# Kernel tuning notes

Measured on AMD Instinct MI355X. Metric: run time of the kernel, lower is better.

The kernel has to match this reference:

```python
import jax, jax.numpy as jnp
import numpy as np

KS = (5, 5, 5)      # dilated_kernel_size (Kd, Kh, Kw)
STRIDE = (1, 1, 1)
PADDING = (2, 2, 2)
GROUPS = 1


def construct_kernel(W, P, ks):
    # W: (oc, ic/g, kc), P: (3, oc, ic/g, kc)
    Kd, Kh, Kw = ks
    lim = jnp.floor_divide(jnp.array([Kd, Kh, Kw], dtype=P.dtype), 2.0)
    Pp = P + lim[:, None, None, None]          # shift to grid coords
    Pf = jnp.floor(Pp)
    R = Pp - Pf                                # fractional parts, (3, oc, ic, kc)
    P1, P2, P3 = Pf[0], Pf[1], Pf[2]
    R1, R2, R3 = R[0], R[1], R[2]
    # trilinear weights factorize per axis. In the torch original:
    #   L (depth axis, Kd)  compares against P1/R1
    #   I (width axis, Kw)  compares against P2/R2
    #   J (height axis, Kh) compares against P3/R3
    gL = jnp.arange(Kd, dtype=P.dtype)[:, None, None, None]
    gJ = jnp.arange(Kh, dtype=P.dtype)[:, None, None, None]
    gI = jnp.arange(Kw, dtype=P.dtype)[:, None, None, None]
    aL = (gL == P1) * (1.0 - R1) + (gL == P1 + 1.0) * R1   # (Kd, oc, ic, kc)
    aJ = (gJ == P3) * (1.0 - R3) + (gJ == P3 + 1.0) * R3   # (Kh, oc, ic, kc)
    aI = (gI == P2) * (1.0 - R2) + (gI == P2 + 1.0) * R2   # (Kw, oc, ic, kc)
    # K[o,c,l,j,i] = sum_k W[o,c,k] * aL[l,o,c,k] * aJ[j,o,c,k] * aI[i,o,c,k]
    K = jnp.einsum('ock,lock,jock,iock->oclji', W, aL, aJ, aI)
    return K  # (oc, ic/g, Kd, Kh, Kw)


def setup_inputs() -> dict:
    key = jax.random.key(0)
    k1, k2, k3, k4 = jax.random.split(key, 4)
    x = jax.random.normal(k1, (2, 32, 16, 32, 32), dtype=jnp.float32)
    weight = jax.random.normal(k2, (64, 32, 16), dtype=jnp.float32) * 0.05
    P = jax.random.normal(k3, (3, 64, 32, 16), dtype=jnp.float32) * 0.5
    bias = jax.random.normal(k4, (64,), dtype=jnp.float32) * 0.05
    return {"x": x, "weight": weight, "P": P, "bias": bias}


def reference(x, weight, P, bias):
    K = construct_kernel(weight, P, KS)
    out = jax.lax.conv_general_dilated(
        x, K,
        window_strides=STRIDE,
        padding=[(p, p) for p in PADDING],
        dimension_numbers=('NCDHW', 'OIDHW', 'NCDHW'),
        feature_group_count=GROUPS,
    )
    return out + bias[None, :, None, None, None]
```

## Files before the change

kernel.cpp:

```cpp
#include <hip/hip_runtime.h>

#define OC 64
#define IC 32
#define KC 16

typedef __attribute__((ext_vector_type(8))) short bf16x8;
typedef __attribute__((ext_vector_type(16))) float f32x16;

__device__ inline unsigned short f2bf(float f) {
    unsigned u = __builtin_bit_cast(unsigned, f);
    unsigned r = (u + 0x7fffu + ((u >> 16) & 1u)) >> 16;
    return (unsigned short)r;
}

__global__ __launch_bounds__(128) void prep(const float* __restrict__ x,
                                            const float* __restrict__ W,
                                            const float* __restrict__ P,
                                            short* __restrict__ xp,
                                            short* __restrict__ Kb) {
    const int b = blockIdx.x;
    if (b < 1440) {
        const int n = b / 720;
        const int rem = b - n * 720;
        const int z = rem / 36;
        const int h = rem - z * 36;
        const int zr = z - 2, hr = h - 2;
        short* orow = xp + (size_t)((n * 20 + z) * 36 + h) * 1152;

        if ((unsigned)zr >= 16u || (unsigned)hr >= 32u) {
            for (int idx = threadIdx.x; idx < 144; idx += 128)
                *reinterpret_cast<float4*>(orow + idx * 8) =
                    make_float4(0.f, 0.f, 0.f, 0.f);
            return;
        }

        __shared__ float sR[32][36];
        const float* xb = x + ((size_t)(n * 32) * 16 + zr) * 1024 + hr * 32;
        for (int idx = threadIdx.x; idx < 32 * 36; idx += 128) {
            const int c = idx / 36;
            const int w = idx - c * 36;
            const int wr = w - 2;
            float v = 0.f;
            if ((unsigned)wr < 32u) v = xb[(size_t)c * 16384 + wr];
            sR[c][w] = v;
        }
        __syncthreads();
        for (int idx = threadIdx.x; idx < 144; idx += 128) {
            const int cg = idx / 36;
            const int w  = idx - cg * 36;
            bf16x8 pk;
            #pragma unroll
            for (int e = 0; e < 8; ++e) pk[e] = (short)f2bf(sR[cg * 8 + e][w]);
            *reinterpret_cast<bf16x8*>(orow + idx * 8) = pk;
        }
    } else {
        const int pair = b - 1440;
        const int o = pair >> 5;
        const int c = pair & 31;
        const int cell = threadIdx.x;
        if (cell >= 125) return;
        const int l = cell / 25;
        const int j = (cell / 5) % 5;
        const int i = cell % 5;
        const float fl = (float)l, fj = (float)j, fi = (float)i;
        const int base = (o * IC + c) * KC;
        float acc = 0.f;
        #pragma unroll
        for (int k = 0; k < KC; ++k) {
            const float w  = W[base + k];
            const float p1 = P[0 * OC * IC * KC + base + k] + 2.0f;
            const float p2 = P[1 * OC * IC * KC + base + k] + 2.0f;
            const float p3 = P[2 * OC * IC * KC + base + k] + 2.0f;
            const float f1 = floorf(p1), r1 = p1 - f1;
            const float f2 = floorf(p2), r2 = p2 - f2;
            const float f3 = floorf(p3), r3 = p3 - f3;
            const float wl = (fl == f1) ? (1.f - r1) : ((fl == f1 + 1.f) ? r1 : 0.f);
            const float wj = (fj == f3) ? (1.f - r3) : ((fj == f3 + 1.f) ? r3 : 0.f);
            const float wi = (fi == f2) ? (1.f - r2) : ((fi == f2 + 1.f) ? r2 : 0.f);
            acc += w * (wl * wj * wi);
        }
        const int og = o >> 5;
        Kb[(size_t)(og * 125 + cell) * 1024 + (c >> 3) * 256 + (o & 31) * 8 + (c & 7)] =
            (short)f2bf(acc);
    }
}

#define ASLOT 25600
#define BBASE 51200
#define BSLOT 13824

__global__ __launch_bounds__(512, 1) void conv_mfma(const short* __restrict__ Kb,
                                                    const short* __restrict__ xp,
                                                    const float* __restrict__ bias,
                                                    float* __restrict__ out) {
    const int sw = (blockIdx.x & 7) * 32 + (blockIdx.x >> 3);
    const int og = sw & 1;
    const int hb = (sw >> 1) & 3;
    const int d  = (sw >> 3) & 15;
    const int n  = sw >> 7;
    const int h0 = hb * 8;

    __shared__ short sL[2 * ASLOT + 2 * BSLOT];

    const int tid  = threadIdx.x;
    const int wv   = tid >> 6;
    const int hp   = wv >> 1;
    const int g    = wv & 1;
    const int lane = tid & 63;
    const int wcol = lane & 31;
    const int hi   = lane >> 5;

    const short* srcA0 = Kb + (size_t)(og * 125) * 1024;
    const short* srcB0 = xp + ((size_t)(n * 20 + d) * 36 + h0) * 1152;

    const int aoff = wcol * 8 + (g * 2 + hi) * 256;
    const int boff = (g * 2 + hi) * 288 + wcol * 8;

    f32x16 acc0, acc1;
    for (int e = 0; e < 16; ++e) { acc0[e] = 0.f; acc1[e] = 0.f; }

    bf16x8 Aq[3][5];
    bf16x8 Bq[3][5];

#define STAGEA(L, BUF)                                                        \
    {                                                                         \
        const short* s_ = srcA0 + (size_t)(L) * 25600;                        \
        short* d_ = sL + (BUF) * ASLOT;                                       \
        _Pragma("unroll")                                                     \
        for (int k_ = 0; k_ < 6; ++k_) {                                      \
            const int t_ = k_ * 512 + tid;                                    \
            __builtin_amdgcn_global_load_lds(                                 \
                (const __attribute__((address_space(1))) unsigned int*)(s_ + t_ * 8), \
                (__attribute__((address_space(3))) unsigned int*)(d_ + t_ * 8), \
                16, 0, 0);                                                    \
        }                                                                     \
        if (tid < 128) {                                                      \
            const int t_ = 3072 + tid;                                        \
            __builtin_amdgcn_global_load_lds(                                 \
                (const __attribute__((address_space(1))) unsigned int*)(s_ + t_ * 8), \
                (__attribute__((address_space(3))) unsigned int*)(d_ + t_ * 8), \
                16, 0, 0);                                                    \
        }                                                                     \
    }

#define STAGEB(L, BUF)                                                        \
    {                                                                         \
        const short* s_ = srcB0 + (size_t)(L) * 41472;                        \
        short* d_ = sL + BBASE + (BUF) * BSLOT;                               \
        _Pragma("unroll")                                                     \
        for (int k_ = 0; k_ < 3; ++k_) {                                      \
            const int t_ = k_ * 512 + tid;                                    \
            __builtin_amdgcn_global_load_lds(                                 \
                (const __attribute__((address_space(1))) unsigned int*)(s_ + t_ * 8), \
                (__attribute__((address_space(3))) unsigned int*)(d_ + t_ * 8), \
                16, 0, 0);                                                    \
        }                                                                     \
        if (tid < 192) {                                                      \
            const int t_ = 1536 + tid;                                        \
            __builtin_amdgcn_global_load_lds(                                 \
                (const __attribute__((address_space(1))) unsigned int*)(s_ + t_ * 8), \
                (__attribute__((address_space(3))) unsigned int*)(d_ + t_ * 8), \
                16, 0, 0);                                                    \
        }                                                                     \
    }

#define LOADA(S, BUF, J)                                                      \
    {                                                                         \
        const short* pa_ = sL + (BUF) * ASLOT + (J) * 5120 + aoff;            \
        _Pragma("unroll")                                                     \
        for (int i_ = 0; i_ < 5; ++i_)                                        \
            Aq[S][i_] = *reinterpret_cast<const bf16x8*>(pa_ + i_ * 1024);    \
    }

#define LOADB(S, BUF, K)                                                      \
    {                                                                         \
        const short* pb_ = sL + BBASE + (BUF) * BSLOT + (2 * hp + (K)) * 1152 + boff; \
        _Pragma("unroll")                                                     \
        for (int i_ = 0; i_ < 5; ++i_)                                        \
            Bq[S][i_] = *reinterpret_cast<const bf16x8*>(pb_ + i_ * 8);       \
    }

#define MFMA_STEP(RA, S0, S1)                                                 \
    {                                                                         \
        __builtin_amdgcn_s_setprio(1);                                        \
        _Pragma("unroll")                                                     \
        for (int i_ = 0; i_ < 5; ++i_) {                                      \
            acc0 = __builtin_amdgcn_mfma_f32_32x32x16_bf16(Aq[RA][i_], Bq[S0][i_], acc0, 0, 0, 0); \
            acc1 = __builtin_amdgcn_mfma_f32_32x32x16_bf16(Aq[RA][i_], Bq[S1][i_], acc1, 0, 0, 0); \
        }                                                                     \
        __builtin_amdgcn_s_setprio(0);                                        \
    }

    STAGEA(0, 0);
    STAGEB(0, 0);
    __syncthreads();

    #pragma unroll
    for (int l = 0; l < 5; ++l) {
        const int buf = l & 1;
        if (l < 4) { STAGEA(l + 1, buf ^ 1); STAGEB(l + 1, buf ^ 1); }
        LOADA(0, buf, 0); LOADA(1, buf, 1);
        LOADB(0, buf, 0); LOADB(1, buf, 1);
        #pragma unroll
        for (int j = 0; j < 5; ++j) {
            if (j < 3) LOADA((j + 2) % 3, buf, j + 2);
            if (j < 4) LOADB((j + 2) % 3, buf, j + 2);
            MFMA_STEP(j % 3, j % 3, (j + 1) % 3);
        }
        if (l < 4) __syncthreads();
    }

#undef STAGEA
#undef STAGEB
#undef LOADA
#undef LOADB
#undef MFMA_STEP

    __syncthreads();
    float* sF = reinterpret_cast<float*>(sL);
    if (g == 1) {
        #pragma unroll
        for (int e = 0; e < 16; ++e) {
            sF[hp * 2048 + e * 64 + lane]        = acc0[e];
            sF[hp * 2048 + (e + 16) * 64 + lane] = acc1[e];
        }
    }
    __syncthreads();
    if (g == 0) {
        const int h = h0 + 2 * hp;
        #pragma unroll
        for (int reg = 0; reg < 16; ++reg) {
            const int o = og * 32 + (reg & 3) + 8 * (reg >> 2) + 4 * hi;
            const float bo = bias[o];
            float* op = out + (((size_t)(n * 64 + o) * 16 + d) * 32 + h) * 32 + wcol;
            op[0]  = acc0[reg] + sF[hp * 2048 + reg * 64 + lane] + bo;
            op[32] = acc1[reg] + sF[hp * 2048 + (reg + 16) * 64 + lane] + bo;
        }
    }
}

extern "C" void kernel_launch(void* const* d_in, const int* in_sizes, int n_in,
                              void* d_out, int out_size, void* d_ws, size_t ws_size,
                              hipStream_t stream) {
    const float* x    = (const float*)d_in[0];
    const float* W    = (const float*)d_in[1];
    const float* P    = (const float*)d_in[2];
    const float* bias = (const float*)d_in[3];
    float* outp = (float*)d_out;

    short* Kb = (short*)d_ws;
    short* xp = (short*)((char*)d_ws + 524288);

    prep<<<1440 + 2048, 128, 0, stream>>>(x, W, P, xp, Kb);
    conv_mfma<<<256, 512, 0, stream>>>(Kb, xp, bias, outp);
}
```

Baseline: 27.02 us.

## Reassign conv waves to 4 output rows with kw-split, batch prep blocks

The conv kernel now gives each wave four output rows with four accumulators and splits the kw taps 3/2 across wave pairs, so each A fragment is reused across four B rows instead of two. The partial sums from four waves are reduced through LDS in the epilogue, and every wave writes one output row. The prep kernel packs two units per 256-thread block, reads x with float4 loads and stages W/P in shared memory. The risks are a larger LDS reduction, more accumulator registers, and an uneven 3/2 kw split between waves.

```diff
diff --git a/kernel.cpp b/kernel.cpp
--- a/kernel.cpp
+++ b/kernel.cpp
@@ -13,75 +13,92 @@
     return (unsigned short)r;
 }
 
-__global__ __launch_bounds__(128) void prep(const float* __restrict__ x,
+__global__ __launch_bounds__(256) void prep(const float* __restrict__ x,
                                             const float* __restrict__ W,
                                             const float* __restrict__ P,
                                             short* __restrict__ xp,
                                             short* __restrict__ Kb) {
-    const int b = blockIdx.x;
-    if (b < 1440) {
-        const int n = b / 720;
-        const int rem = b - n * 720;
+    __shared__ float sR[2][32][36];
+    __shared__ float sWP[2][64];
+    const int tid = threadIdx.x;
+    const int u   = tid >> 7;
+    const int ut  = tid & 127;
+    const int b   = blockIdx.x;
+
+    if (b < 720) {
+        const int ub = b * 2 + u;
+        const int n = ub / 720;
+        const int rem = ub - n * 720;
         const int z = rem / 36;
         const int h = rem - z * 36;
         const int zr = z - 2, hr = h - 2;
         short* orow = xp + (size_t)((n * 20 + z) * 36 + h) * 1152;
-
-        if ((unsigned)zr >= 16u || (unsigned)hr >= 32u) {
-            for (int idx = threadIdx.x; idx < 144; idx += 128)
+        const bool edge = ((unsigned)zr >= 16u) || ((unsigned)hr >= 32u);
+
+        if (!edge) {
+            const float* xb = x + ((size_t)(n * 32) * 16 + zr) * 1024 + hr * 32;
+            #pragma unroll
+            for (int k = 0; k < 2; ++k) {
+                const int id = ut + k * 128;
+                const int c = id >> 3, w4 = id & 7;
+                const float4 v = *reinterpret_cast<const float4*>(xb + c * 16384 + w4 * 4);
+                float* dst = &sR[u][c][2 + w4 * 4];
+                *reinterpret_cast<float2*>(dst)     = make_float2(v.x, v.y);
+                *reinterpret_cast<float2*>(dst + 2) = make_float2(v.z, v.w);
+            }
+            {
+                const int c = ut >> 2, wz = ut & 3;
+                const int w = (wz < 2) ? wz : 32 + wz;
+                sR[u][c][w] = 0.f;
+            }
+        }
+        __syncthreads();
+        if (edge) {
+            for (int idx = ut; idx < 144; idx += 128)
                 *reinterpret_cast<float4*>(orow + idx * 8) =
                     make_float4(0.f, 0.f, 0.f, 0.f);
-            return;
-        }
-
-        __shared__ float sR[32][36];
-        const float* xb = x + ((size_t)(n * 32) * 16 + zr) * 1024 + hr * 32;
-        for (int idx = threadIdx.x; idx < 32 * 36; idx += 128) {
-            const int c = idx / 36;
-            const int w = idx - c * 36;
-            const int wr = w - 2;
-            float v = 0.f;
-            if ((unsigned)wr < 32u) v = xb[(size_t)c * 16384 + wr];
-            sR[c][w] = v;
-        }
-        __syncthreads();
-        for (int idx = threadIdx.x; idx < 144; idx += 128) {
-            const int cg = idx / 36;
-            const int w  = idx - cg * 36;
-            bf16x8 pk;
-            #pragma unroll
-            for (int e = 0; e < 8; ++e) pk[e] = (short)f2bf(sR[cg * 8 + e][w]);
-            *reinterpret_cast<bf16x8*>(orow + idx * 8) = pk;
+        } else {
+            for (int idx = ut; idx < 144; idx += 128) {
+                const int cg = idx / 36;
+                const int w  = idx - cg * 36;
+                bf16x8 pk;
+                #pragma unroll
+                for (int e = 0; e < 8; ++e) pk[e] = (short)f2bf(sR[u][cg * 8 + e][w]);
+                *reinterpret_cast<bf16x8*>(orow + idx * 8) = pk;
+            }
         }
     } else {
-        const int pair = b - 1440;
-        const int o = pair >> 5;
-        const int c = pair & 31;
-        const int cell = threadIdx.x;
-        if (cell >= 125) return;
-        const int l = cell / 25;
-        const int j = (cell / 5) % 5;
-        const int i = cell % 5;
-        const float fl = (float)l, fj = (float)j, fi = (float)i;
-        const int base = (o * IC + c) * KC;
-        float acc = 0.f;
-        #pragma unroll
-        for (int k = 0; k < KC; ++k) {
-            const float w  = W[base + k];
-            const float p1 = P[0 * OC * IC * KC + base + k] + 2.0f;
-            const float p2 = P[1 * OC * IC * KC + base + k] + 2.0f;
-            const float p3 = P[2 * OC * IC * KC + base + k] + 2.0f;
-            const float f1 = floorf(p1), r1 = p1 - f1;
-            const float f2 = floorf(p2), r2 = p2 - f2;
-            const float f3 = floorf(p3), r3 = p3 - f3;
-            const float wl = (fl == f1) ? (1.f - r1) : ((fl == f1 + 1.f) ? r1 : 0.f);
-            const float wj = (fj == f3) ? (1.f - r3) : ((fj == f3 + 1.f) ? r3 : 0.f);
-            const float wi = (fi == f2) ? (1.f - r2) : ((fi == f2 + 1.f) ? r2 : 0.f);
-            acc += w * (wl * wj * wi);
+        const int pair = (b - 720) * 2 + u;
+        if (ut < 64)
+            sWP[u][ut] = (ut < 16) ? W[pair * 16 + ut]
+                                   : P[((ut >> 4) - 1) * 32768 + pair * 16 + (ut & 15)];
+        __syncthreads();
+        if (ut < 125) {
+            const int cell = ut;
+            const int l = cell / 25;
+            const int j = (cell / 5) % 5;
+            const int i = cell % 5;
+            const float fl = (float)l, fj = (float)j, fi = (float)i;
+            float acc = 0.f;
+            #pragma unroll
+            for (int k = 0; k < KC; ++k) {
+                const float w  = sWP[u][k];
+                const float p1 = sWP[u][16 + k] + 2.0f;
+                const float p2 = sWP[u][32 + k] + 2.0f;
+                const float p3 = sWP[u][48 + k] + 2.0f;
+                const float f1 = floorf(p1), r1 = p1 - f1;
+                const float f2 = floorf(p2), r2 = p2 - f2;
+                const float f3 = floorf(p3), r3 = p3 - f3;
+                const float wl = (fl == f1) ? (1.f - r1) : ((fl == f1 + 1.f) ? r1 : 0.f);
+                const float wj = (fj == f3) ? (1.f - r3) : ((fj == f3 + 1.f) ? r3 : 0.f);
+                const float wi = (fi == f2) ? (1.f - r2) : ((fi == f2 + 1.f) ? r2 : 0.f);
+                acc += w * (wl * wj * wi);
+            }
+            const int o = pair >> 5, c = pair & 31;
+            const int og = o >> 5;
+            Kb[(size_t)(og * 125 + cell) * 1024 + (c >> 3) * 256 + (o & 31) * 8 + (c & 7)] =
+                (short)f2bf(acc);
         }
-        const int og = o >> 5;
-        Kb[(size_t)(og * 125 + cell) * 1024 + (c >> 3) * 256 + (o & 31) * 8 + (c & 7)] =
-            (short)f2bf(acc);
     }
 }
 
@@ -89,7 +106,7 @@
 #define BBASE 51200
 #define BSLOT 13824
 
-__global__ __launch_bounds__(512, 1) void conv_mfma(const short* __restrict__ Kb,
+__global__ __launch_bounds__(512, 2) void conv_mfma(const short* __restrict__ Kb,
                                                     const short* __restrict__ xp,
                                                     const float* __restrict__ bias,
                                                     float* __restrict__ out) {
@@ -104,23 +121,26 @@
 
     const int tid  = threadIdx.x;
     const int wv   = tid >> 6;
-    const int hp   = wv >> 1;
-    const int g    = wv & 1;
     const int lane = tid & 63;
     const int wcol = lane & 31;
     const int hi   = lane >> 5;
+    const int hp   = wv >> 2;
+    const int g    = (wv >> 1) & 1;
+    const int s    = (wv ^ (wv >> 2)) & 1;
 
     const short* srcA0 = Kb + (size_t)(og * 125) * 1024;
     const short* srcB0 = xp + ((size_t)(n * 20 + d) * 36 + h0) * 1152;
 
     const int aoff = wcol * 8 + (g * 2 + hi) * 256;
     const int boff = (g * 2 + hi) * 288 + wcol * 8;
-
-    f32x16 acc0, acc1;
-    for (int e = 0; e < 16; ++e) { acc0[e] = 0.f; acc1[e] = 0.f; }
-
-    bf16x8 Aq[3][5];
-    bf16x8 Bq[3][5];
+    const int rb   = 4 * hp;
+
+    f32x16 ac0, ac1, ac2, ac3;
+    #pragma unroll
+    for (int e = 0; e < 16; ++e) { ac0[e] = 0.f; ac1[e] = 0.f; ac2[e] = 0.f; ac3[e] = 0.f; }
+
+    bf16x8 Aq[2][3];
+    bf16x8 Bq[5][3];
 
 #define STAGEA(L, BUF)                                                        \
     {                                                                         \
@@ -164,78 +184,91 @@
         }                                                                     \
     }
 
-#define LOADA(S, BUF, J)                                                      \
-    {                                                                         \
-        const short* pa_ = sL + (BUF) * ASLOT + (J) * 5120 + aoff;            \
-        _Pragma("unroll")                                                     \
-        for (int i_ = 0; i_ < 5; ++i_)                                        \
-            Aq[S][i_] = *reinterpret_cast<const bf16x8*>(pa_ + i_ * 1024);    \
-    }
-
-#define LOADB(S, BUF, K)                                                      \
-    {                                                                         \
-        const short* pb_ = sL + BBASE + (BUF) * BSLOT + (2 * hp + (K)) * 1152 + boff; \
-        _Pragma("unroll")                                                     \
-        for (int i_ = 0; i_ < 5; ++i_)                                        \
-            Bq[S][i_] = *reinterpret_cast<const bf16x8*>(pb_ + i_ * 8);       \
-    }
-
-#define MFMA_STEP(RA, S0, S1)                                                 \
+#define LOADA(PAR, BUF, J, I0, NI)                                            \
+    {                                                                         \
+        const short* pa_ = sL + (BUF) * ASLOT + ((J) * 5 + (I0)) * 1024 + aoff; \
+        _Pragma("unroll")                                                     \
+        for (int ii = 0; ii < (NI); ++ii)                                     \
+            Aq[PAR][ii] = *reinterpret_cast<const bf16x8*>(pa_ + ii * 1024);  \
+    }
+
+#define LOADB(SLOT, BUF, RW, I0, NI)                                          \
+    {                                                                         \
+        const short* pb_ = sL + BBASE + (BUF) * BSLOT + (rb + (RW)) * 1152 + boff + (I0) * 8; \
+        _Pragma("unroll")                                                     \
+        for (int ii = 0; ii < (NI); ++ii)                                     \
+            Bq[SLOT][ii] = *reinterpret_cast<const bf16x8*>(pb_ + ii * 8);    \
+    }
+
+#define MFMA_STEP(J, NI)                                                      \
     {                                                                         \
         __builtin_amdgcn_s_setprio(1);                                        \
         _Pragma("unroll")                                                     \
-        for (int i_ = 0; i_ < 5; ++i_) {                                      \
-            acc0 = __builtin_amdgcn_mfma_f32_32x32x16_bf16(Aq[RA][i_], Bq[S0][i_], acc0, 0, 0, 0); \
-            acc1 = __builtin_amdgcn_mfma_f32_32x32x16_bf16(Aq[RA][i_], Bq[S1][i_], acc1, 0, 0, 0); \
+        for (int ii = 0; ii < (NI); ++ii) {                                   \
+            const bf16x8 a_ = Aq[(J) & 1][ii];                                \
+            ac0 = __builtin_amdgcn_mfma_f32_32x32x16_bf16(a_, Bq[(J) % 5][ii], ac0, 0, 0, 0);       \
+            ac1 = __builtin_amdgcn_mfma_f32_32x32x16_bf16(a_, Bq[((J) + 1) % 5][ii], ac1, 0, 0, 0); \
+            ac2 = __builtin_amdgcn_mfma_f32_32x32x16_bf16(a_, Bq[((J) + 2) % 5][ii], ac2, 0, 0, 0); \
+            ac3 = __builtin_amdgcn_mfma_f32_32x32x16_bf16(a_, Bq[((J) + 3) % 5][ii], ac3, 0, 0, 0); \
         }                                                                     \
         __builtin_amdgcn_s_setprio(0);                                        \
     }
 
-    STAGEA(0, 0);
-    STAGEB(0, 0);
-    __syncthreads();
-
-    #pragma unroll
-    for (int l = 0; l < 5; ++l) {
-        const int buf = l & 1;
-        if (l < 4) { STAGEA(l + 1, buf ^ 1); STAGEB(l + 1, buf ^ 1); }
-        LOADA(0, buf, 0); LOADA(1, buf, 1);
-        LOADB(0, buf, 0); LOADB(1, buf, 1);
-        #pragma unroll
-        for (int j = 0; j < 5; ++j) {
-            if (j < 3) LOADA((j + 2) % 3, buf, j + 2);
-            if (j < 4) LOADB((j + 2) % 3, buf, j + 2);
-            MFMA_STEP(j % 3, j % 3, (j + 1) % 3);
-        }
-        if (l < 4) __syncthreads();
-    }
+#define MAIN(I0, NI)                                                          \
+    {                                                                         \
+        STAGEA(0, 0); STAGEB(0, 0);                                           \
+        __syncthreads();                                                      \
+        _Pragma("unroll")                                                     \
+        for (int l = 0; l < 5; ++l) {                                         \
+            const int buf = l & 1;                                            \
+            if (l < 4) { STAGEA(l + 1, buf ^ 1); STAGEB(l + 1, buf ^ 1); }    \
+            LOADA(0, buf, 0, I0, NI);                                         \
+            LOADB(0, buf, 0, I0, NI);                                         \
+            LOADB(1, buf, 1, I0, NI);                                         \
+            LOADB(2, buf, 2, I0, NI);                                         \
+            LOADB(3, buf, 3, I0, NI);                                         \
+            _Pragma("unroll")                                                 \
+            for (int j = 0; j < 5; ++j) {                                     \
+                if (j < 4) {                                                  \
+                    LOADA((j + 1) & 1, buf, j + 1, I0, NI);                   \
+                    LOADB((j + 4) % 5, buf, j + 4, I0, NI);                   \
+                }                                                             \
+                MFMA_STEP(j, NI);                                             \
+            }                                                                 \
+            if (l < 4) __syncthreads();                                       \
+        }                                                                     \
+    }
+
+    if (s == 0) { MAIN(0, 3) } else { MAIN(3, 2) }
 
 #undef STAGEA
 #undef STAGEB
 #undef LOADA
 #undef LOADB
 #undef MFMA_STEP
+#undef MAIN
 
     __syncthreads();
     float* sF = reinterpret_cast<float*>(sL);
-    if (g == 1) {
+    const int wbase = (g * 2 + s) * 2 + hp;
+#define WR(R, A)                                                              \
+    { _Pragma("unroll")                                                       \
+      for (int e = 0; e < 16; ++e)                                            \
+          sF[((wbase * 4 + (R)) * 16 + e) * 64 + lane] = A[e]; }
+    WR(0, ac0) WR(1, ac1) WR(2, ac2) WR(3, ac3)
+#undef WR
+    __syncthreads();
+
+    const int hpR = wv >> 2, rR = wv & 3;
+    const int h = h0 + wv;
+    #pragma unroll
+    for (int e = 0; e < 16; ++e) {
+        float v = 0.f;
         #pragma unroll
-        for (int e = 0; e < 16; ++e) {
-            sF[hp * 2048 + e * 64 + lane]        = acc0[e];
-            sF[hp * 2048 + (e + 16) * 64 + lane] = acc1[e];
-        }
-    }
-    __syncthreads();
-    if (g == 0) {
-        const int h = h0 + 2 * hp;
-        #pragma unroll
-        for (int reg = 0; reg < 16; ++reg) {
-            const int o = og * 32 + (reg & 3) + 8 * (reg >> 2) + 4 * hi;
-            const float bo = bias[o];
-            float* op = out + (((size_t)(n * 64 + o) * 16 + d) * 32 + h) * 32 + wcol;
-            op[0]  = acc0[reg] + sF[hp * 2048 + reg * 64 + lane] + bo;
-            op[32] = acc1[reg] + sF[hp * 2048 + (reg + 16) * 64 + lane] + bo;
-        }
+        for (int q = 0; q < 4; ++q)
+            v += sF[(((q * 2 + hpR) * 4 + rR) * 16 + e) * 64 + lane];
+        const int o = og * 32 + (e & 3) + 8 * (e >> 2) + 4 * hi;
+        out[((size_t)(n * 64 + o) * 16 + d) * 1024 + h * 32 + wcol] = v + bias[o];
     }
 }
 
@@ -251,6 +284,6 @@
     short* Kb = (short*)d_ws;
     short* xp = (short*)((char*)d_ws + 524288);
 
-    prep<<<1440 + 2048, 128, 0, stream>>>(x, W, P, xp, Kb);
+    prep<<<1744, 256, 0, stream>>>(x, W, P, xp, Kb);
     conv_mfma<<<256, 512, 0, stream>>>(Kb, xp, bias, outp);
 }
```

After: 26.14 us. -3.2%, faster.
